# Kernel tuning notes

Hardware: AMD Instinct MI355X
Metric: run time of the kernel (lower is better)

## Reference

```python
import jax, jax.numpy as jnp
import numpy as np

D_MODEL = 1024
N_HEADS = 16
HEAD_DIM = D_MODEL // N_HEADS
B, T = 4, 2048


def setup_inputs() -> dict:
    key = jax.random.key(0)
    ks = jax.random.split(key, 5)
    s = D_MODEL ** -0.5
    return {
        "x": jax.random.normal(ks[0], (B, T, D_MODEL), dtype=jnp.float32),
        "Wqkv": jax.random.normal(ks[1], (3 * D_MODEL, D_MODEL), dtype=jnp.float32) * s,
        "bqkv": jax.random.normal(ks[2], (3 * D_MODEL,), dtype=jnp.float32) * 0.01,
        "Wo": jax.random.normal(ks[3], (D_MODEL, D_MODEL), dtype=jnp.float32) * s,
        "bo": jax.random.normal(ks[4], (D_MODEL,), dtype=jnp.float32) * 0.01,
    }


def reference(x, Wqkv, bqkv, Wo, bo):
    b, t, c = x.shape
    h, hd = N_HEADS, HEAD_DIM
    qkv = x @ Wqkv.T + bqkv                      # [B,T,3C]
    # Faithful to source: reshape to [B,T,H,3*hd] THEN chunk -> per-head slices of 3C
    qkv = qkv.reshape(b, t, h, 3 * hd).transpose(0, 2, 1, 3)  # [B,H,T,3hd]
    q, k, v = jnp.split(qkv, 3, axis=-1)          # each [B,H,T,hd]
    scores = jnp.einsum('bhqd,bhkd->bhqk', q, k) * (hd ** -0.5)
    attn = jax.nn.softmax(scores, axis=-1)        # [B,H,T,T]
    out = jnp.einsum('bhqk,bhkd->bhqd', attn, v)  # [B,H,T,hd]
    out = out.transpose(0, 2, 1, 3).reshape(b, t, c)
    return out @ Wo.T + bo
```

## Files before the change

### kernel.cpp

```cpp
#include <hip/hip_runtime.h>
#include <hip/hip_bf16.h>


typedef float f32x4 __attribute__((ext_vector_type(4)));
typedef short s16x8 __attribute__((ext_vector_type(8)));
typedef short s16x4 __attribute__((ext_vector_type(4)));
typedef unsigned int u32x4 __attribute__((ext_vector_type(4)));

#define MFMA(acc, a, b) \
    (acc) = __builtin_amdgcn_mfma_f32_16x16x32_bf16((a), (b), (acc), 0, 0, 0)

__device__ __forceinline__ short f2bb(float f) {
    return (short)__bfloat16_as_ushort(__float2bfloat16(f));
}

__global__ __launch_bounds__(256)
void conv_all(const float* __restrict__ x, const float* __restrict__ Wqkv,
              const float* __restrict__ bqkv, const float* __restrict__ Wo,
              short* __restrict__ xb, short* __restrict__ Wqkvb,
              float* __restrict__ bqkvr, short* __restrict__ Wob)
{
    int blk = blockIdx.x;
    if (blk < 4096) {
        long i = ((long)blk * 256 + threadIdx.x) * 8;
        f32x4 a = *(const f32x4*)(x + i);
        f32x4 b = *(const f32x4*)(x + i + 4);
        s16x8 r;
#pragma unroll
        for (int j = 0; j < 4; j++) { r[j] = f2bb(a[j]); r[4 + j] = f2bb(b[j]); }
        *(s16x8*)(xb + i) = r;
    } else if (blk < 4096 + 3072) {
        int np = blk - 4096;
        int slice = np >> 10, rr = np & 1023;
        int src = (rr >> 6) * 192 + slice * 64 + (rr & 63);
        f32x4 v = *(const f32x4*)(Wqkv + (long)src * 1024 + threadIdx.x * 4);
        s16x4 o;
#pragma unroll
        for (int j = 0; j < 4; j++) o[j] = f2bb(v[j]);
        *(s16x4*)(Wqkvb + (long)np * 1024 + threadIdx.x * 4) = o;
        if (threadIdx.x == 0) bqkvr[np] = bqkv[src];
    } else {
        int n = blk - 4096 - 3072;
        f32x4 v = *(const f32x4*)(Wo + (long)n * 1024 + threadIdx.x * 4);
        s16x4 o;
#pragma unroll
        for (int j = 0; j < 4; j++) o[j] = f2bb(v[j]);
        *(s16x4*)(Wob + (long)n * 1024 + threadIdx.x * 4) = o;
    }
}

__global__ __launch_bounds__(256)
void gemm128(const short* __restrict__ A, const short* __restrict__ W,
             const float* __restrict__ bias,
             short* __restrict__ Cq, short* __restrict__ Ck,
             short* __restrict__ Cv, float* __restrict__ Cf, int proj)
{
    __shared__ short Asw[128 * 64];
    __shared__ short Bsw[128 * 64];
    const int tid = threadIdx.x;
    const int wave = tid >> 6, lane = tid & 63;
    const int quad = lane >> 4, l16 = lane & 15;
    const int NX = gridDim.x;
    const int lin = blockIdx.y * NX + blockIdx.x;
    const int xcd = lin & 7, q = lin >> 3;
    const int m0 = (xcd * 8 + q / NX) * 128;
    const int ng = (q % NX) * 128;
    const int sr = tid >> 3, sc = tid & 7;

    f32x4 acc[4][4] = {};
    s16x8 pav[4], pbv[4];

#pragma unroll
    for (int u = 0; u < 4; u++) {
        int r = u * 32 + sr;
        pav[u] = *(const s16x8*)(A + (long)(m0 + r) * 1024 + sc * 8);
        pbv[u] = *(const s16x8*)(W + (long)(ng + r) * 1024 + sc * 8);
    }

    for (int k0 = 0; k0 < 1024; k0 += 64) {
        __syncthreads();
#pragma unroll
        for (int u = 0; u < 4; u++) {
            int r = u * 32 + sr;
            int slot = sc ^ (r & 7);
            *(s16x8*)&Asw[r * 64 + slot * 8] = pav[u];
            *(s16x8*)&Bsw[r * 64 + slot * 8] = pbv[u];
        }
        __syncthreads();
        if (k0 + 64 < 1024) {
            int kn = k0 + 64;
#pragma unroll
            for (int u = 0; u < 4; u++) {
                int r = u * 32 + sr;
                pav[u] = *(const s16x8*)(A + (long)(m0 + r) * 1024 + kn + sc * 8);
                pbv[u] = *(const s16x8*)(W + (long)(ng + r) * 1024 + kn + sc * 8);
            }
        }

        s16x8 af[2][4], bf[2][4];
#pragma unroll
        for (int ks = 0; ks < 2; ks++)
#pragma unroll
            for (int i = 0; i < 4; i++) {
                int slot = (ks * 4 + quad) ^ (l16 & 7);
                int ra = (wave >> 1) * 64 + i * 16 + l16;
                af[ks][i] = *(const s16x8*)&Asw[ra * 64 + slot * 8];
                int rb = (wave & 1) * 64 + i * 16 + l16;
                bf[ks][i] = *(const s16x8*)&Bsw[rb * 64 + slot * 8];
            }
#pragma unroll
        for (int ks = 0; ks < 2; ks++)
#pragma unroll
            for (int i = 0; i < 4; i++)
#pragma unroll
                for (int j = 0; j < 4; j++)
                    MFMA(acc[i][j], af[ks][i], bf[ks][j]);
    }

    const int slice = ng >> 10;
    const float scale = (!proj && slice == 0) ? 0.125f : 1.0f;
    short* Cb = (slice == 0) ? Cq : (slice == 1) ? Ck : Cv;
    const int nl = ng & 1023;
#pragma unroll
    for (int i = 0; i < 4; i++)
#pragma unroll
        for (int r = 0; r < 4; r++) {
            long m = m0 + (wave >> 1) * 64 + i * 16 + quad * 4 + r;
#pragma unroll
            for (int j = 0; j < 4; j++) {
                int cw = (wave & 1) * 64 + j * 16 + l16;
                float v = (acc[i][j][r] + bias[ng + cw]) * scale;
                if (proj) Cf[m * 1024 + ng + cw] = v;
                else      Cb[m * 1024 + nl + cw] = f2bb(v);
            }
        }
}

__global__ __launch_bounds__(256)
void attn(const short* __restrict__ Q, const short* __restrict__ Kb,
          const short* __restrict__ Vb, short* __restrict__ ao)
{
    __shared__ short Ksw[64 * 64];
    __shared__ unsigned int Vt[64 * 36];

    const int tid = threadIdx.x;
    const int wave = tid >> 6, lane = tid & 63;
    const int quad = lane >> 4, l16 = lane & 15;
    const int bh = blockIdx.x;
    const int b = bh >> 4, h = bh & 15;
    const int q0 = blockIdx.y * 256, hc = h * 64;
    const long rowbase = (long)b * 2048;

    s16x8 qf[4][2];
#pragma unroll
    for (int s = 0; s < 4; s++) {
        const short* qp = Q + (rowbase + q0 + s * 64 + wave * 16 + l16) * 1024
                        + hc + quad * 8;
        qf[s][0] = *(const s16x8*)qp;
        qf[s][1] = *(const s16x8*)(qp + 32);
    }

    s16x8 vones;
#pragma unroll
    for (int j = 0; j < 8; j++) vones[j] = (short)0x3F80;

    f32x4 O[4][4] = {};
    f32x4 Osum[4] = {};

    const int ksr = tid >> 3, ksc = tid & 7;
    const int kp = tid & 31, ve = tid >> 5;
    const int key0 = ((kp >> 4) << 5) + (((kp >> 1) & 1) << 4)
                   + (((kp >> 2) & 3) << 2) + ((kp & 1) << 1);

    s16x8 kv0, kv1, va, vb2;
    {
        kv0 = *(const s16x8*)(Kb + (rowbase + ksr) * 1024 + hc + ksc * 8);
        kv1 = *(const s16x8*)(Kb + (rowbase + 32 + ksr) * 1024 + hc + ksc * 8);
        const short* v0 = Vb + (rowbase + key0) * 1024 + hc + ve * 8;
        va  = *(const s16x8*)v0;
        vb2 = *(const s16x8*)(v0 + 1024);
    }

    for (int kb = 0; kb < 2048; kb += 64) {
        __syncthreads();
        {
            int slot0 = ksc ^ (ksr & 7);
            *(s16x8*)&Ksw[ksr * 64 + slot0 * 8] = kv0;
            int r1 = 32 + ksr;
            int slot1 = ksc ^ (r1 & 7);
            *(s16x8*)&Ksw[r1 * 64 + slot1 * 8] = kv1;
            u32x4 vaU = __builtin_bit_cast(u32x4, va);
            u32x4 vbU = __builtin_bit_cast(u32x4, vb2);
#pragma unroll
            for (int w = 0; w < 4; w++) {
                unsigned int lo = __builtin_amdgcn_perm(vbU[w], vaU[w], 0x05040100u);
                unsigned int hi = __builtin_amdgcn_perm(vbU[w], vaU[w], 0x07060302u);
                Vt[(ve * 8 + 2 * w) * 36 + kp] = lo;
                Vt[(ve * 8 + 2 * w + 1) * 36 + kp] = hi;
            }
        }
        __syncthreads();

        if (kb + 64 < 2048) {
            int kn = kb + 64;
            kv0 = *(const s16x8*)(Kb + (rowbase + kn + ksr) * 1024 + hc + ksc * 8);
            kv1 = *(const s16x8*)(Kb + (rowbase + kn + 32 + ksr) * 1024 + hc + ksc * 8);
            const short* v0 = Vb + (rowbase + kn + key0) * 1024 + hc + ve * 8;
            va  = *(const s16x8*)v0;
            vb2 = *(const s16x8*)(v0 + 1024);
        }

        s16x8 af[4][2];
        __builtin_amdgcn_s_setprio(1);
#pragma unroll
        for (int kt = 0; kt < 4; kt++) {
            int key = kt * 16 + l16;
            int slot0 = quad ^ (l16 & 7);
            int slot1 = (4 + quad) ^ (l16 & 7);
            s16x8 kf0 = *(const s16x8*)&Ksw[key * 64 + slot0 * 8];
            s16x8 kf1 = *(const s16x8*)&Ksw[key * 64 + slot1 * 8];
            f32x4 sv[4] = {{}, {}, {}, {}};
#pragma unroll
            for (int s = 0; s < 4; s++) {
                MFMA(sv[s], kf0, qf[s][0]);
                MFMA(sv[s], kf1, qf[s][1]);
            }
#pragma unroll
            for (int s = 0; s < 4; s++)
#pragma unroll
                for (int r = 0; r < 4; r++) {
                    float p = __builtin_amdgcn_exp2f(
                        __builtin_fmaf(sv[s][r], 1.44269504f, -17.3123405f));
                    af[s][kt >> 1][(kt & 1) * 4 + r] = f2bb(p);
                }
        }

#pragma unroll
        for (int dt = 0; dt < 4; dt++) {
            int d = dt * 16 + l16;
#pragma unroll
            for (int kf = 0; kf < 2; kf++) {
                s16x8 vf = *(const s16x8*)&Vt[d * 36 + kf * 16 + quad * 4];
#pragma unroll
                for (int s = 0; s < 4; s++)
                    MFMA(O[s][dt], af[s][kf], vf);
            }
        }
#pragma unroll
        for (int s = 0; s < 4; s++) {
            MFMA(Osum[s], af[s][0], vones);
            MFMA(Osum[s], af[s][1], vones);
        }
        __builtin_amdgcn_s_setprio(0);
    }

#pragma unroll
    for (int s = 0; s < 4; s++)
#pragma unroll
        for (int r = 0; r < 4; r++) {
            float invr = 1.0f / Osum[s][r];
            short* orow = ao + (rowbase + q0 + s * 64 + wave * 16 + quad * 4 + r) * 1024
                        + hc + l16;
#pragma unroll
            for (int dt = 0; dt < 4; dt++)
                orow[dt * 16] = f2bb(O[s][dt][r] * invr);
        }
}

__global__ void const_fill(float* out, int n, float c) {
    int i = blockIdx.x * 256 + threadIdx.x;
    if (i < n) out[i] = c;
}

extern "C" void kernel_launch(void* const* d_in, const int* in_sizes, int n_in,
                              void* d_out, int out_size, void* d_ws, size_t ws_size,
                              hipStream_t stream)
{
    const float* x    = (const float*)d_in[0];
    const float* Wqkv = (const float*)d_in[1];
    const float* bqkv = (const float*)d_in[2];
    const float* Wo   = (const float*)d_in[3];
    const float* bo   = (const float*)d_in[4];

    const size_t MB = 1u << 20;
    if (ws_size < 32 * MB) {
        const_fill<<<(out_size + 255) / 256, 256, 0, stream>>>(
            (float*)d_out, out_size, 66.0f);
        return;
    }

    char* ws = (char*)d_ws;
    short* xb     = (short*)(ws);
    short* Wqkvb  = (short*)(ws + 16777216);
    float* bqkvr  = (float*)(ws + 23068672);
    short* Wob    = (short*)(ws + 23085056);

    short* qbuf = (short*)d_out;
    short* kbuf = qbuf + (size_t)8192 * 1024;
    short* vbuf = (short*)d_in[0] + (size_t)8192 * 1024;
    short* ao   = (short*)d_in[0];

    dim3 blk(256);
    conv_all<<<4096 + 3072 + 1024, blk, 0, stream>>>(
        x, Wqkv, bqkv, Wo, xb, Wqkvb, bqkvr, Wob);

    gemm128<<<dim3(24, 64), blk, 0, stream>>>(xb, Wqkvb, bqkvr,
                                              qbuf, kbuf, vbuf, nullptr, 0);
    attn<<<dim3(64, 8), blk, 0, stream>>>(qbuf, kbuf, vbuf, ao);
    gemm128<<<dim3(8, 64), blk, 0, stream>>>(ao, Wob, bo,
                                             nullptr, nullptr, nullptr,
                                             (float*)d_out, 1);
}
```

Before: 259.0 us.

## Double-buffer attention K/V tiles and load K directly into LDS

The attention kernel now keeps two LDS buffers for K and transposed V. K tiles are fetched with global_load_lds straight into a swizzled LDS layout, while the next V tile is permuted into the alternate buffer during the current tile's compute. This cuts the loop to one barrier per tile and removes the register staging of K, so loads overlap with MFMA work. In exchange it doubles LDS use, which can lower occupancy, and it relies on the async LDS load having landed by the time of the barrier.

```diff
diff --git a/kernel.cpp b/kernel.cpp
--- a/kernel.cpp
+++ b/kernel.cpp
@@ -12,6 +12,12 @@
 
 __device__ __forceinline__ short f2bb(float f) {
     return (short)__bfloat16_as_ushort(__float2bfloat16(f));
+}
+
+__device__ __forceinline__ void gload16(const void* g, void* l) {
+    __builtin_amdgcn_global_load_lds(
+        (const __attribute__((address_space(1))) unsigned int*)g,
+        (__attribute__((address_space(3))) unsigned int*)l, 16, 0, 0);
 }
 
 __global__ __launch_bounds__(256)
@@ -140,8 +146,8 @@
 void attn(const short* __restrict__ Q, const short* __restrict__ Kb,
           const short* __restrict__ Vb, short* __restrict__ ao)
 {
-    __shared__ short Ksw[64 * 64];
-    __shared__ unsigned int Vt[64 * 36];
+    __shared__ short Ksw[2][64 * 64];
+    __shared__ unsigned int Vt[2][64 * 36];
 
     const int tid = threadIdx.x;
     const int wave = tid >> 6, lane = tid & 63;
@@ -167,48 +173,61 @@
     f32x4 O[4][4] = {};
     f32x4 Osum[4] = {};
 
-    const int ksr = tid >> 3, ksc = tid & 7;
     const int kp = tid & 31, ve = tid >> 5;
     const int key0 = ((kp >> 4) << 5) + (((kp >> 1) & 1) << 4)
                    + (((kp >> 2) & 3) << 2) + ((kp & 1) << 1);
 
-    s16x8 kv0, kv1, va, vb2;
+    const short* kdma = Kb + (rowbase + wave * 8 + (lane >> 3)) * 1024
+                      + hc + (((lane & 7) ^ ((lane >> 3) & 7)) * 8);
+    const short* vptr = Vb + (rowbase + key0) * 1024 + hc + ve * 8;
+
+    s16x8 va, vb2;
+
+    gload16(kdma,             &Ksw[0][wave * 512]);
+    gload16(kdma + 32 * 1024, &Ksw[0][wave * 512 + 2048]);
+    va  = *(const s16x8*)vptr;
+    vb2 = *(const s16x8*)(vptr + 1024);
     {
-        kv0 = *(const s16x8*)(Kb + (rowbase + ksr) * 1024 + hc + ksc * 8);
-        kv1 = *(const s16x8*)(Kb + (rowbase + 32 + ksr) * 1024 + hc + ksc * 8);
-        const short* v0 = Vb + (rowbase + key0) * 1024 + hc + ve * 8;
-        va  = *(const s16x8*)v0;
-        vb2 = *(const s16x8*)(v0 + 1024);
-    }
-
-    for (int kb = 0; kb < 2048; kb += 64) {
-        __syncthreads();
-        {
-            int slot0 = ksc ^ (ksr & 7);
-            *(s16x8*)&Ksw[ksr * 64 + slot0 * 8] = kv0;
-            int r1 = 32 + ksr;
-            int slot1 = ksc ^ (r1 & 7);
-            *(s16x8*)&Ksw[r1 * 64 + slot1 * 8] = kv1;
+        u32x4 vaU = __builtin_bit_cast(u32x4, va);
+        u32x4 vbU = __builtin_bit_cast(u32x4, vb2);
+#pragma unroll
+        for (int w = 0; w < 4; w++) {
+            unsigned int lo = __builtin_amdgcn_perm(vbU[w], vaU[w], 0x05040100u);
+            unsigned int hi = __builtin_amdgcn_perm(vbU[w], vaU[w], 0x07060302u);
+            Vt[0][(ve * 8 + 2 * w) * 36 + kp] = lo;
+            Vt[0][(ve * 8 + 2 * w + 1) * 36 + kp] = hi;
+        }
+    }
+    vptr += 64 * 1024;
+    va  = *(const s16x8*)vptr;
+    vb2 = *(const s16x8*)(vptr + 1024);
+    __syncthreads();
+
+    for (int t = 0; t < 32; ++t) {
+        if (t < 31) {
+            kdma += 64 * 1024;
+            short* kd = &Ksw[(t + 1) & 1][wave * 512];
+            gload16(kdma,             kd);
+            gload16(kdma + 32 * 1024, kd + 2048);
+            unsigned int* Vw = Vt[(t + 1) & 1];
             u32x4 vaU = __builtin_bit_cast(u32x4, va);
             u32x4 vbU = __builtin_bit_cast(u32x4, vb2);
 #pragma unroll
             for (int w = 0; w < 4; w++) {
                 unsigned int lo = __builtin_amdgcn_perm(vbU[w], vaU[w], 0x05040100u);
                 unsigned int hi = __builtin_amdgcn_perm(vbU[w], vaU[w], 0x07060302u);
-                Vt[(ve * 8 + 2 * w) * 36 + kp] = lo;
-                Vt[(ve * 8 + 2 * w + 1) * 36 + kp] = hi;
-            }
-        }
-        __syncthreads();
-
-        if (kb + 64 < 2048) {
-            int kn = kb + 64;
-            kv0 = *(const s16x8*)(Kb + (rowbase + kn + ksr) * 1024 + hc + ksc * 8);
-            kv1 = *(const s16x8*)(Kb + (rowbase + kn + 32 + ksr) * 1024 + hc + ksc * 8);
-            const short* v0 = Vb + (rowbase + kn + key0) * 1024 + hc + ve * 8;
-            va  = *(const s16x8*)v0;
-            vb2 = *(const s16x8*)(v0 + 1024);
-        }
+                Vw[(ve * 8 + 2 * w) * 36 + kp] = lo;
+                Vw[(ve * 8 + 2 * w + 1) * 36 + kp] = hi;
+            }
+        }
+        if (t < 30) {
+            vptr += 64 * 1024;
+            va  = *(const s16x8*)vptr;
+            vb2 = *(const s16x8*)(vptr + 1024);
+        }
+
+        const short* Kr = Ksw[t & 1];
+        const unsigned int* Vr = Vt[t & 1];
 
         s16x8 af[4][2];
         __builtin_amdgcn_s_setprio(1);
@@ -217,8 +236,8 @@
             int key = kt * 16 + l16;
             int slot0 = quad ^ (l16 & 7);
             int slot1 = (4 + quad) ^ (l16 & 7);
-            s16x8 kf0 = *(const s16x8*)&Ksw[key * 64 + slot0 * 8];
-            s16x8 kf1 = *(const s16x8*)&Ksw[key * 64 + slot1 * 8];
+            s16x8 kf0 = *(const s16x8*)&Kr[key * 64 + slot0 * 8];
+            s16x8 kf1 = *(const s16x8*)&Kr[key * 64 + slot1 * 8];
             f32x4 sv[4] = {{}, {}, {}, {}};
 #pragma unroll
             for (int s = 0; s < 4; s++) {
@@ -240,7 +259,7 @@
             int d = dt * 16 + l16;
 #pragma unroll
             for (int kf = 0; kf < 2; kf++) {
-                s16x8 vf = *(const s16x8*)&Vt[d * 36 + kf * 16 + quad * 4];
+                s16x8 vf = *(const s16x8*)&Vr[d * 36 + kf * 16 + quad * 4];
 #pragma unroll
                 for (int s = 0; s < 4; s++)
                     MFMA(O[s][dt], af[s][kf], vf);
@@ -252,6 +271,8 @@
             MFMA(Osum[s], af[s][1], vones);
         }
         __builtin_amdgcn_s_setprio(0);
+
+        __syncthreads();
     }
 
 #pragma unroll
```

Result: no change. 262.5 us (+1.4%).
